# Performance work log

Hardware: AMD Instinct MI355X
Metric: run time of the kernel (lower is better)

Reference implementation:

```python
import jax, jax.numpy as jnp
import numpy as np

# Hyperparameters (from init_kwargs)
D_MODEL = 1024
D_STATE = 64
HEADDIM = 64
MIMO_RANK = 2
CHUNK = 128
EXPAND = 2
D_INNER = EXPAND * D_MODEL            # 2048
NHEADS = D_INNER // HEADDIM           # 32
G = MIMO_RANK * D_STATE               # effective state channels per head = 128
D_CONV = 4
D_XBC = D_INNER + 2 * NHEADS * G      # conv channels
D_IN_PROJ = 2 * D_INNER + 2 * NHEADS * G + NHEADS  # [z, x, B, C, dt]


def rmsnorm(x, w, eps=1e-5):
    return x * w * jax.lax.rsqrt(jnp.mean(x * x, axis=-1, keepdims=True) + eps)


def setup_inputs() -> dict:
    key = jax.random.key(0)
    ks = jax.random.split(key, 8)
    B, L = 2, 2048
    x = jax.random.normal(ks[0], (B, L, D_MODEL), jnp.float32)
    norm_w = jnp.ones((D_MODEL,), jnp.float32)
    in_proj_w = jax.random.normal(ks[1], (D_IN_PROJ, D_MODEL), jnp.float32) * 0.02
    conv_w = jax.random.normal(ks[2], (D_XBC, D_CONV), jnp.float32) * 0.2
    conv_b = jnp.zeros((D_XBC,), jnp.float32)
    dt_bias = jax.random.uniform(ks[3], (NHEADS,), jnp.float32, minval=-4.0, maxval=-1.0)
    A_log = jnp.log(jax.random.uniform(ks[4], (NHEADS,), jnp.float32, minval=1.0, maxval=8.0))
    D_skip = jnp.ones((NHEADS,), jnp.float32)
    gnorm_w = jnp.ones((D_INNER,), jnp.float32)
    out_proj_w = jax.random.normal(ks[5], (D_MODEL, D_INNER), jnp.float32) * 0.02
    return dict(x=x, norm_w=norm_w, in_proj_w=in_proj_w, conv_w=conv_w, conv_b=conv_b,
                dt_bias=dt_bias, A_log=A_log, D_skip=D_skip, gnorm_w=gnorm_w,
                out_proj_w=out_proj_w)


def _mamba3(u, in_proj_w, conv_w, conv_b, dt_bias, A_log, D_skip, gnorm_w, out_proj_w):
    B, L, _ = u.shape
    H, P = NHEADS, HEADDIM
    nc = L // CHUNK

    zxbcdt = u @ in_proj_w.T                                   # (B,L,D_IN_PROJ)
    z, xbc, dt_raw = jnp.split(zxbcdt, [D_INNER, D_INNER + D_XBC], axis=-1)

    # causal depthwise conv (width D_CONV) + SiLU on [x, B, C]
    xp = jnp.pad(xbc, ((0, 0), (D_CONV - 1, 0), (0, 0)))
    conv = conv_b + sum(xp[:, k:k + L, :] * conv_w[:, k] for k in range(D_CONV))
    xbc = jax.nn.silu(conv)
    xh, Bm, Cm = jnp.split(xbc, [D_INNER, D_INNER + H * G], axis=-1)

    Xc = xh.reshape(B, nc, CHUNK, H, P)
    Bc = Bm.reshape(B, nc, CHUNK, H, G)
    Cc = Cm.reshape(B, nc, CHUNK, H, G)

    dt = jax.nn.softplus(dt_raw + dt_bias)                     # (B,L,H), positive
    A = -jnp.exp(A_log)                                        # (H,), negative
    dtc = dt.reshape(B, nc, CHUNK, H)
    a = dtc * A                                                # log decay, (B,nc,cs,H)
    cum = jnp.cumsum(a, axis=2)                                # inclusive cumsum within chunk

    # intra-chunk (quadratic, causal) part
    cumT = cum.transpose(0, 1, 3, 2)                           # (B,nc,H,cs)
    diff = cumT[..., :, None] - cumT[..., None, :]             # cum_l - cum_s
    mask = jnp.tril(jnp.ones((CHUNK, CHUNK), bool))
    decay = jnp.where(mask, jnp.exp(jnp.where(mask, diff, 0.0)), 0.0)
    dtT = dtc.transpose(0, 1, 3, 2)                            # (B,nc,H,cs)
    scores = jnp.einsum('bclhg,bcshg->bchls', Cc, Bc) * decay * dtT[:, :, :, None, :]
    Y_intra = jnp.einsum('bchls,bcshp->bclhp', scores, Xc)

    # inter-chunk state recurrence
    w = jnp.exp(cum[:, :, -1:, :] - cum) * dtc                 # (B,nc,cs,H)
    S = jnp.einsum('bcshg,bcshp->bchgp', Bc * w[..., None], Xc)  # chunk states
    dlast = jnp.exp(cum[:, :, -1, :])                          # (B,nc,H) total chunk decay

    def step(carry, inp):
        dl, s = inp
        return dl[:, :, None, None] * carry + s, carry

    init = jnp.zeros((B, H, G, P), u.dtype)
    _, Hprev = jax.lax.scan(step, init, (dlast.transpose(1, 0, 2), S.transpose(1, 0, 2, 3, 4)))
    Hprev = Hprev.transpose(1, 0, 2, 3, 4)                     # (B,nc,H,G,P) state before chunk
    Y_inter = jnp.einsum('bclhg,bchgp->bclhp', Cc * jnp.exp(cum)[..., None], Hprev)

    y = (Y_intra + Y_inter + D_skip[:, None] * Xc).reshape(B, L, D_INNER)
    y = rmsnorm(y * jax.nn.silu(z), gnorm_w)                   # gated RMSNorm
    return y @ out_proj_w.T


def reference(x, norm_w, in_proj_w, conv_w, conv_b, dt_bias, A_log, D_skip, gnorm_w, out_proj_w):
    # pre-norm residual wrapper
    return x + _mamba3(rmsnorm(x, norm_w), in_proj_w, conv_w, conv_b,
                       dt_bias, A_log, D_skip, gnorm_w, out_proj_w)
```

## Files before the change

kernel.cpp:

```cpp
#include <hip/hip_runtime.h>

typedef unsigned short u16;
typedef __attribute__((ext_vector_type(8))) short bf16x8;
typedef __attribute__((ext_vector_type(4))) float f32x4;

#define MFMA16(a,b,c) __builtin_amdgcn_mfma_f32_16x16x32_bf16(a,b,c,0,0,0)

#define DMODEL   1024
#define DINNER   2048
#define NHEADS   32
#define HEADDIM  64
#define GDIM     128
#define DXBC     10240
#define DPROJ    12320
#define CHUNK_L  128
#define NCHUNK   16
#define NROWS    4096

__device__ __forceinline__ float b2f(u16 u){ return __uint_as_float(((unsigned)u)<<16); }
__device__ __forceinline__ u16 f2b(float f){
  unsigned u = __float_as_uint(f);
  u += 0x7fffu + ((u>>16)&1u);
  return (u16)(u>>16);
}

__device__ __forceinline__ void gload_lds16(const void* g, void* l){
  __builtin_amdgcn_global_load_lds(
      (const __attribute__((address_space(1))) unsigned int*)g,
      (__attribute__((address_space(3))) unsigned int*)l, 16, 0, 0);
}

__global__ void k_f32_to_bf16(const float* __restrict__ src, u16* __restrict__ dst, int n){
  int i = blockIdx.x*blockDim.x + threadIdx.x;
  int stride = gridDim.x*blockDim.x;
  int n4 = n >> 2;
  for (int j=i; j<n4; j+=stride){
    float4 v = reinterpret_cast<const float4*>(src)[j];
    uint2 o;
    o.x = (unsigned)f2b(v.x) | ((unsigned)f2b(v.y)<<16);
    o.y = (unsigned)f2b(v.z) | ((unsigned)f2b(v.w)<<16);
    reinterpret_cast<uint2*>(dst)[j] = o;
  }
}

__global__ __launch_bounds__(256) void k_rmsnorm_in(const float* __restrict__ x,
                                                    const float* __restrict__ w,
                                                    u16* __restrict__ u){
  int row = blockIdx.x, tid = threadIdx.x;
  float4 v = reinterpret_cast<const float4*>(x + (size_t)row*DMODEL)[tid];
  float ss = v.x*v.x + v.y*v.y + v.z*v.z + v.w*v.w;
  #pragma unroll
  for (int off=32; off>0; off>>=1) ss += __shfl_down(ss, off, 64);
  __shared__ float red[4];
  if ((tid&63)==0) red[tid>>6] = ss;
  __syncthreads();
  float tot = red[0]+red[1]+red[2]+red[3];
  float sc = rsqrtf(tot/(float)DMODEL + 1e-5f);
  float4 wv = reinterpret_cast<const float4*>(w)[tid];
  uint2 o;
  o.x = (unsigned)f2b(v.x*wv.x*sc) | ((unsigned)f2b(v.y*wv.y*sc)<<16);
  o.y = (unsigned)f2b(v.z*wv.z*sc) | ((unsigned)f2b(v.w*wv.w*sc)<<16);
  reinterpret_cast<uint2*>(u + (size_t)row*DMODEL)[tid] = o;
}

__global__ __launch_bounds__(512) void k_gemm1_8p(const u16* __restrict__ A,
                                                  const u16* __restrict__ W,
                                                  u16* __restrict__ zb,
                                                  u16* __restrict__ xbc){
  __shared__ __align__(16) u16 lds[65536];
  const int tid  = threadIdx.x;
  const int lane = tid & 63, w = tid >> 6;
  const int wr = w >> 2, wc = w & 3;
  int bid = blockIdx.x;
  int xcd = bid & 7, g = bid >> 3;
  int st  = xcd*6 + (g >> 4);
  int wi  = g & 15;
  int tm  = (st/12)*4 + (wi>>2);
  int tn  = (st%12)*4 + (wi&3);
  const int m0 = tm*256, n0 = tn*256;

  const int srow = w*8 + (lane>>3);
  const int scol = ((lane&7) ^ ((lane>>3)&7))*8;
  const u16* aS = A + (size_t)(m0 + srow)*DMODEL + scol;
  const u16* bS = W + (size_t)(n0 + srow)*DMODEL + scol;
  const int ldsw = w*512;

  const int rr = lane & 15, gq = lane >> 4;

  f32x4 acc[8][4];
  #pragma unroll
  for (int i=0;i<8;i++)
    #pragma unroll
    for (int j=0;j<4;j++) acc[i][j] = (f32x4){0,0,0,0};

  auto SU_A = [&](int kt, int j){
    gload_lds16(aS + (size_t)(j*64)*DMODEL + kt*64,
                lds + (kt&1)*32768 + j*4096 + ldsw);
  };
  auto SU_B = [&](int kt, int j){
    gload_lds16(bS + (size_t)(j*64)*DMODEL + kt*64,
                lds + (kt&1)*32768 + 16384 + j*4096 + ldsw);
  };

  SU_A(0,0); SU_A(0,2); SU_B(0,0); SU_B(0,2); SU_B(0,1); SU_B(0,3); SU_A(0,1); SU_A(0,3);
  asm volatile("s_waitcnt vmcnt(2)" ::: "memory");
  __builtin_amdgcn_s_barrier();
  __builtin_amdgcn_sched_barrier(0);

  for (int kt = 0; kt < 16; ++kt){
    const u16* bufA = lds + (kt&1)*32768;
    const u16* bufB = bufA + 16384;
    const bool stg = (kt < 15);
    bf16x8 af[4][2], bw0[2][2], bw1[2][2];

    auto RDA = [&](int ti, int ks)->bf16x8{
      int r = wr*128 + ti*16 + rr;
      int s = (ks*4 + gq) ^ (rr & 7);
      return *(const bf16x8*)&bufA[r*64 + s*8];
    };
    auto RDB = [&](int tj, int ks)->bf16x8{
      int r = wc*64 + tj*16 + rr;
      int s = (ks*4 + gq) ^ (rr & 7);
      return *(const bf16x8*)&bufB[r*64 + s*8];
    };

    #pragma unroll
    for (int ti=0;ti<4;ti++){ af[ti][0]=RDA(ti,0); af[ti][1]=RDA(ti,1); }
    #pragma unroll
    for (int tj=0;tj<2;tj++){ bw0[tj][0]=RDB(tj,0); bw0[tj][1]=RDB(tj,1); }
    if (stg){ SU_A(kt+1,0); SU_A(kt+1,2); }
    __builtin_amdgcn_s_barrier();
    asm volatile("s_waitcnt lgkmcnt(0)" ::: "memory");
    __builtin_amdgcn_sched_barrier(0);
    __builtin_amdgcn_s_setprio(1);
    #pragma unroll
    for (int ti=0;ti<4;ti++)
      #pragma unroll
      for (int tj=0;tj<2;tj++){
        acc[ti][tj] = MFMA16(af[ti][0], bw0[tj][0], acc[ti][tj]);
        acc[ti][tj] = MFMA16(af[ti][1], bw0[tj][1], acc[ti][tj]);
      }
    __builtin_amdgcn_s_setprio(0);
    __builtin_amdgcn_s_barrier();

    #pragma unroll
    for (int tj=0;tj<2;tj++){ bw1[tj][0]=RDB(tj+2,0); bw1[tj][1]=RDB(tj+2,1); }
    if (stg){ SU_B(kt+1,0); SU_B(kt+1,2); }
    __builtin_amdgcn_s_barrier();
    asm volatile("s_waitcnt lgkmcnt(0)" ::: "memory");
    __builtin_amdgcn_sched_barrier(0);
    __builtin_amdgcn_s_setprio(1);
    #pragma unroll
    for (int ti=0;ti<4;ti++)
      #pragma unroll
      for (int tj=0;tj<2;tj++){
        acc[ti][tj+2] = MFMA16(af[ti][0], bw1[tj][0], acc[ti][tj+2]);
        acc[ti][tj+2] = MFMA16(af[ti][1], bw1[tj][1], acc[ti][tj+2]);
      }
    __builtin_amdgcn_s_setprio(0);
    if (stg) asm volatile("s_waitcnt vmcnt(4)" ::: "memory");
    else     asm volatile("s_waitcnt vmcnt(0)" ::: "memory");
    __builtin_amdgcn_s_barrier();

    #pragma unroll
    for (int ti=0;ti<4;ti++){ af[ti][0]=RDA(ti+4,0); af[ti][1]=RDA(ti+4,1); }
    if (stg){ SU_B(kt+1,1); SU_B(kt+1,3); }
    __builtin_amdgcn_s_barrier();
    asm volatile("s_waitcnt lgkmcnt(0)" ::: "memory");
    __builtin_amdgcn_sched_barrier(0);
    __builtin_amdgcn_s_setprio(1);
    #pragma unroll
    for (int ti=0;ti<4;ti++)
      #pragma unroll
      for (int tj=0;tj<2;tj++){
        acc[4+ti][tj] = MFMA16(af[ti][0], bw0[tj][0], acc[4+ti][tj]);
        acc[4+ti][tj] = MFMA16(af[ti][1], bw0[tj][1], acc[4+ti][tj]);
      }
    __builtin_amdgcn_s_setprio(0);
    __builtin_amdgcn_s_barrier();

    if (stg){ SU_A(kt+1,1); SU_A(kt+1,3); }
    __builtin_amdgcn_s_barrier();
    __builtin_amdgcn_sched_barrier(0);
    __builtin_amdgcn_s_setprio(1);
    #pragma unroll
    for (int ti=0;ti<4;ti++)
      #pragma unroll
      for (int tj=0;tj<2;tj++){
        acc[4+ti][tj+2] = MFMA16(af[ti][0], bw1[tj][0], acc[4+ti][tj+2]);
        acc[4+ti][tj+2] = MFMA16(af[ti][1], bw1[tj][1], acc[4+ti][tj+2]);
      }
    __builtin_amdgcn_s_setprio(0);
    if (stg){
      asm volatile("s_waitcnt vmcnt(2)" ::: "memory");
      __builtin_amdgcn_s_barrier();
      __builtin_amdgcn_sched_barrier(0);
    }
  }

  const int row0 = m0 + wr*128 + (lane>>4)*4;
  const int colb = wc*64 + (lane&15);
  if (tn >= 8){
    const int cb = n0 - DINNER;
    #pragma unroll
    for (int ti=0;ti<8;ti++)
      #pragma unroll
      for (int tj=0;tj<4;tj++)
        #pragma unroll
        for (int q=0;q<4;q++)
          xbc[(size_t)(row0 + ti*16 + q)*DXBC + cb + colb + tj*16] = f2b(acc[ti][tj][q]);
  } else {
    #pragma unroll
    for (int ti=0;ti<8;ti++)
      #pragma unroll
      for (int tj=0;tj<4;tj++)
        #pragma unroll
        for (int q=0;q<4;q++)
          zb[(size_t)(row0 + ti*16 + q)*DINNER + n0 + colb + tj*16] = f2b(acc[ti][tj][q]);
  }
}

__global__ __launch_bounds__(256) void k_gemm_dt(const u16* __restrict__ A,
                                                 const u16* __restrict__ W,
                                                 float* __restrict__ dtraw){
  const int lane = threadIdx.x & 63, wv = threadIdx.x >> 6;
  const int m0 = blockIdx.x*32;
  const int n0 = DINNER + DXBC;
  const int r  = lane & 15;
  const int kb = (lane>>4)*8;
  const int k0 = wv*256;
  const u16* a0p = A + (size_t)(m0 + r)*DMODEL + k0 + kb;
  const u16* a1p = a0p + 16*DMODEL;
  const u16* b0p = W + (size_t)(n0 + r)*DMODEL + k0 + kb;
  const u16* b1p = b0p + 16*DMODEL;
  f32x4 acc00={0,0,0,0}, acc01={0,0,0,0}, acc10={0,0,0,0}, acc11={0,0,0,0};
  #pragma unroll
  for (int k=0;k<256;k+=32){
    bf16x8 a0 = *(const bf16x8*)(a0p + k);
    bf16x8 a1 = *(const bf16x8*)(a1p + k);
    bf16x8 b0 = *(const bf16x8*)(b0p + k);
    bf16x8 b1 = *(const bf16x8*)(b1p + k);
    acc00 = MFMA16(a0,b0,acc00);
    acc01 = MFMA16(a0,b1,acc01);
    acc10 = MFMA16(a1,b0,acc10);
    acc11 = MFMA16(a1,b1,acc11);
  }
  __shared__ float part[4][1024];
  int rowb = (lane>>4)*4, col = lane&15;
  #pragma unroll
  for (int rr=0; rr<4; rr++){
    part[wv][(rowb+rr)*32 + col]         = acc00[rr];
    part[wv][(rowb+rr)*32 + col+16]      = acc01[rr];
    part[wv][(rowb+16+rr)*32 + col]      = acc10[rr];
    part[wv][(rowb+16+rr)*32 + col+16]   = acc11[rr];
  }
  __syncthreads();
  int idx = threadIdx.x*4;
  #pragma unroll
  for (int q=0;q<4;q++){
    int i = idx+q;
    dtraw[(size_t)m0*NHEADS + i] = part[0][i]+part[1][i]+part[2][i]+part[3][i];
  }
}

__global__ __launch_bounds__(256) void k_conv(const u16* __restrict__ xbc,
                                              const float* __restrict__ cw,
                                              const float* __restrict__ cb,
                                              u16* __restrict__ xh,
                                              u16* __restrict__ Bm,
                                              u16* __restrict__ Cm){
  int c  = (blockIdx.x*256 + threadIdx.x)*2;
  int row0 = blockIdx.y*8;
  int l0 = row0 & 2047;
  float4 wa = reinterpret_cast<const float4*>(cw)[c];
  float4 wb = reinterpret_cast<const float4*>(cw)[c+1];
  float cba = cb[c], cbb = cb[c+1];
  float a3=0,a2=0,a1=0, b3=0,b2=0,b1=0;
  auto loadpair = [&](int rw, float& fa, float& fb){
    unsigned v = *(const unsigned*)&xbc[(size_t)rw*DXBC + c];
    fa = b2f((u16)v); fb = b2f((u16)(v>>16));
  };
  if (l0 >= 3){
    loadpair(row0-3, a3,b3); loadpair(row0-2, a2,b2); loadpair(row0-1, a1,b1);
  }
  #pragma unroll
  for (int i=0;i<8;i++){
    float a0,b0; loadpair(row0+i, a0,b0);
    float sa = cba + a3*wa.x + a2*wa.y + a1*wa.z + a0*wa.w;
    float sb = cbb + b3*wb.x + b2*wb.y + b1*wb.z + b0*wb.w;
    sa = sa/(1.f+expf(-sa)); sb = sb/(1.f+expf(-sb));
    unsigned o = (unsigned)f2b(sa) | ((unsigned)f2b(sb)<<16);
    int rw = row0 + i;
    if (c < DINNER)            *(unsigned*)&xh[(size_t)rw*DINNER + c] = o;
    else if (c < DINNER+4096)  *(unsigned*)&Bm[(size_t)rw*4096 + (c-DINNER)] = o;
    else                       *(unsigned*)&Cm[(size_t)rw*4096 + (c-DINNER-4096)] = o;
    a3=a2; a2=a1; a1=a0; b3=b2; b2=b1; b1=b0;
  }
}

__global__ __launch_bounds__(128) void k_dtscan(const float* __restrict__ dtraw,
                                                const float* __restrict__ dt_bias,
                                                const float* __restrict__ A_log,
                                                float* __restrict__ dtT,
                                                float* __restrict__ cumT){
  int blk = blockIdx.x;
  int h   = blk & 31;
  int bc  = blk >> 5;
  int s   = threadIdx.x;
  int row = bc*128 + s;
  float xv = dtraw[(size_t)row*NHEADS + h] + dt_bias[h];
  float dt = (xv > 20.f) ? xv : log1pf(expf(xv));
  float a  = dt * (-expf(A_log[h]));
  __shared__ float lds[128];
  lds[s] = a; __syncthreads();
  #pragma unroll
  for (int off=1; off<128; off<<=1){
    float t = (s>=off) ? lds[s-off] : 0.f;
    __syncthreads();
    lds[s] += t;
    __syncthreads();
  }
  dtT[(size_t)blk*128 + s]  = dt;
  cumT[(size_t)blk*128 + s] = lds[s];
}

__global__ __launch_bounds__(256) void k_states(const u16* __restrict__ Bm,
                                                const u16* __restrict__ xh,
                                                const float* __restrict__ dtT,
                                                const float* __restrict__ cumT,
                                                u16* __restrict__ S){
  int blk = blockIdx.x;
  int h = blk & 31, bc = blk >> 5;
  __shared__ __align__(16) u16 Bw[128][136];
  __shared__ __align__(16) u16 XT[64][136];
  __shared__ float cum[128], dtv[128];
  int tid = threadIdx.x;
  if (tid < 128){ cum[tid] = cumT[(size_t)blk*128+tid]; dtv[tid] = dtT[(size_t)blk*128+tid]; }
  __syncthreads();
  float clast = cum[127];
  #pragma unroll
  for (int it=0; it<8; ++it){
    int s  = it*16 + (tid>>4);
    int g8 = (tid&15)*8;
    uint4 v = *(const uint4*)&Bm[(size_t)(bc*128+s)*4096 + h*128 + g8];
    float w = expf(clast - cum[s]) * dtv[s];
    const u16* pv = (const u16*)&v;
    #pragma unroll
    for (int j=0;j<8;j++) Bw[g8+j][s] = f2b(b2f(pv[j]) * w);
  }
  #pragma unroll
  for (int it=0; it<8; ++it){
    int s  = it*16 + (tid>>4);
    int p4 = (tid&15)*4;
    uint2 v = *(const uint2*)&xh[(size_t)(bc*128+s)*DINNER + h*64 + p4];
    const u16* pv = (const u16*)&v;
    #pragma unroll
    for (int j=0;j<4;j++) XT[p4+j][s] = pv[j];
  }
  __syncthreads();
  int lane = tid & 63, wv = tid >> 6;
  int r = lane & 15, kb = (lane>>4)*8;
  f32x4 acc[2][4];
  #pragma unroll
  for (int i=0;i<2;i++)
    #pragma unroll
    for (int j=0;j<4;j++) acc[i][j] = (f32x4){0,0,0,0};
  #pragma unroll
  for (int k=0;k<128;k+=32){
    bf16x8 a0 = *(const bf16x8*)&Bw[wv*32 + r][k+kb];
    bf16x8 a1 = *(const bf16x8*)&Bw[wv*32 + 16 + r][k+kb];
    #pragma unroll
    for (int tj=0;tj<4;tj++){
      bf16x8 bb = *(const bf16x8*)&XT[tj*16 + r][k+kb];
      acc[0][tj] = MFMA16(a0,bb,acc[0][tj]);
      acc[1][tj] = MFMA16(a1,bb,acc[1][tj]);
    }
  }
  u16* Sp = S + (size_t)blk*8192;
  int g0 = wv*32 + (lane>>4)*4, p0 = lane&15;
  #pragma unroll
  for (int ti=0;ti<2;ti++)
    #pragma unroll
    for (int tj=0;tj<4;tj++)
      #pragma unroll
      for (int rr=0;rr<4;rr++)
        Sp[(g0 + ti*16 + rr)*64 + tj*16 + p0] = f2b(acc[ti][tj][rr]);
}

__global__ __launch_bounds__(256) void k_scan(const u16* __restrict__ S,
                                              const float* __restrict__ cumT,
                                              u16* __restrict__ Hp){
  int slice = blockIdx.x & 3;
  int bh = blockIdx.x >> 2;
  int b = bh >> 5, h = bh & 31;
  int e0 = slice*2048 + threadIdx.x*8;
  float c8[8];
  #pragma unroll
  for (int j=0;j<8;j++) c8[j] = 0.f;
  for (int c=0;c<NCHUNK;c++){
    int blk = (b*16+c)*32 + h;
    float dl = expf(cumT[(size_t)blk*128 + 127]);
    uint4 sv = *(const uint4*)&S[(size_t)blk*8192 + e0];
    const u16* sp = (const u16*)&sv;
    uint4 o; u16* op = (u16*)&o;
    #pragma unroll
    for (int j=0;j<8;j++) op[j] = f2b(c8[j]);
    *reinterpret_cast<uint4*>(&Hp[(size_t)blk*8192 + e0]) = o;
    #pragma unroll
    for (int j=0;j<8;j++) c8[j] = dl*c8[j] + b2f(sp[j]);
  }
}

__global__ __launch_bounds__(256) void k_intra(const u16* __restrict__ Cm,
                                               const u16* __restrict__ Bm,
                                               const u16* __restrict__ xh,
                                               const u16* __restrict__ Hp,
                                               const float* __restrict__ dtT,
                                               const float* __restrict__ cumT,
                                               const float* __restrict__ Dskip,
                                               u16* __restrict__ yh){
  int blk = blockIdx.x;
  int h = blk & 31, bc = blk >> 5;
  __shared__ __align__(16) u16 Cl[128][136];
  __shared__ __align__(16) u16 Bl[128][136];
  __shared__ __align__(16) u16 XT[64][136];
  __shared__ __align__(16) u16 HT[64][136];
  __shared__ float cum[128], dtv[128];
  int tid = threadIdx.x;
  if (tid < 128){ cum[tid] = cumT[(size_t)blk*128+tid]; dtv[tid] = dtT[(size_t)blk*128+tid]; }
  #pragma unroll
  for (int it=0; it<8; ++it){
    int rw = it*16 + (tid>>4);
    int g8 = (tid&15)*8;
    *(uint4*)&Cl[rw][g8] = *(const uint4*)&Cm[(size_t)(bc*128+rw)*4096 + h*128 + g8];
    *(uint4*)&Bl[rw][g8] = *(const uint4*)&Bm[(size_t)(bc*128+rw)*4096 + h*128 + g8];
  }
  #pragma unroll
  for (int it=0; it<8; ++it){
    int s  = it*16 + (tid>>4);
    int p4 = (tid&15)*4;
    uint2 v = *(const uint2*)&xh[(size_t)(bc*128+s)*DINNER + h*64 + p4];
    const u16* pv = (const u16*)&v;
    #pragma unroll
    for (int j=0;j<4;j++) XT[p4+j][s] = pv[j];
  }
  #pragma unroll
  for (int it=0; it<8; ++it){
    int g  = it*16 + (tid>>4);
    int p4 = (tid&15)*4;
    uint2 v = *(const uint2*)&Hp[(size_t)blk*8192 + g*64 + p4];
    const u16* pv = (const u16*)&v;
    #pragma unroll
    for (int j=0;j<4;j++) HT[p4+j][g] = pv[j];
  }
  __syncthreads();
  int lane = tid & 63, wv = tid >> 6;
  int r = lane & 15, kb = (lane>>4)*8;
  const int tjmax = 2*wv + 1;

  f32x4 p1[2][8];
  #pragma unroll
  for (int i=0;i<2;i++)
    #pragma unroll
    for (int j=0;j<8;j++) p1[i][j] = (f32x4){0,0,0,0};
  #pragma unroll
  for (int k=0;k<128;k+=32){
    bf16x8 a0 = *(const bf16x8*)&Cl[wv*32 + r][k+kb];
    bf16x8 a1 = *(const bf16x8*)&Cl[wv*32 + 16 + r][k+kb];
    #pragma unroll
    for (int tj=0;tj<8;tj++){
      if (tj > tjmax) continue;
      bf16x8 bb = *(const bf16x8*)&Bl[tj*16 + r][k+kb];
      p1[0][tj] = MFMA16(a0,bb,p1[0][tj]);
      p1[1][tj] = MFMA16(a1,bb,p1[1][tj]);
    }
  }
  __syncthreads();
  int row0 = wv*32 + (lane>>4)*4;
  #pragma unroll
  for (int ti=0;ti<2;ti++)
    #pragma unroll
    for (int tj=0;tj<8;tj++)
      #pragma unroll
      for (int rr=0;rr<4;rr++){
        int l = row0 + ti*16 + rr;
        int s = tj*16 + (lane&15);
        float v = p1[ti][tj][rr];
        v = (s <= l) ? v * expf(cum[l]-cum[s]) * dtv[s] : 0.f;
        Bl[l][s] = f2b(v);
      }
  __syncthreads();

  f32x4 y[2][4];
  #pragma unroll
  for (int i=0;i<2;i++)
    #pragma unroll
    for (int j=0;j<4;j++) y[i][j] = (f32x4){0,0,0,0};
  #pragma unroll
  for (int k=0;k<128;k+=32){
    bf16x8 a0 = *(const bf16x8*)&Cl[wv*32 + r][k+kb];
    bf16x8 a1 = *(const bf16x8*)&Cl[wv*32 + 16 + r][k+kb];
    #pragma unroll
    for (int tj=0;tj<4;tj++){
      bf16x8 bb = *(const bf16x8*)&HT[tj*16 + r][k+kb];
      y[0][tj] = MFMA16(a0,bb,y[0][tj]);
      y[1][tj] = MFMA16(a1,bb,y[1][tj]);
    }
  }
  #pragma unroll
  for (int ti=0;ti<2;ti++){
    #pragma unroll
    for (int rr=0;rr<4;rr++){
      float e = expf(cum[row0 + ti*16 + rr]);
      #pragma unroll
      for (int tj=0;tj<4;tj++) y[ti][tj][rr] *= e;
    }
  }
  #pragma unroll
  for (int k=0;k<128;k+=32){
    bf16x8 a0 = *(const bf16x8*)&Bl[wv*32 + r][k+kb];
    bf16x8 a1 = *(const bf16x8*)&Bl[wv*32 + 16 + r][k+kb];
    #pragma unroll
    for (int tj=0;tj<4;tj++){
      bf16x8 bb = *(const bf16x8*)&XT[tj*16 + r][k+kb];
      y[0][tj] = MFMA16(a0,bb,y[0][tj]);
      y[1][tj] = MFMA16(a1,bb,y[1][tj]);
    }
  }
  float Dh = Dskip[h];
  #pragma unroll
  for (int ti=0;ti<2;ti++)
    #pragma unroll
    for (int tj=0;tj<4;tj++)
      #pragma unroll
      for (int rr=0;rr<4;rr++){
        int l = row0 + ti*16 + rr;
        int p = tj*16 + (lane&15);
        float xv = b2f(XT[p][l]);
        yh[(size_t)(bc*128 + l)*DINNER + h*64 + p] = f2b(y[ti][tj][rr] + Dh*xv);
      }
}

__global__ __launch_bounds__(256) void k_gate(const u16* __restrict__ yh,
                                              const u16* __restrict__ zb,
                                              const float* __restrict__ gw,
                                              u16* __restrict__ out){
  int row = blockIdx.x, tid = threadIdx.x;
  const uint4 yv = reinterpret_cast<const uint4*>(yh + (size_t)row*DINNER)[tid];
  const uint4 zv = reinterpret_cast<const uint4*>(zb + (size_t)row*DINNER)[tid];
  const unsigned* yp = (const unsigned*)&yv;
  const unsigned* zp = (const unsigned*)&zv;
  float t[8]; float ss = 0.f;
  #pragma unroll
  for (int i=0;i<4;i++){
    float y0 = b2f((u16)yp[i]), y1 = b2f((u16)(yp[i]>>16));
    float z0 = b2f((u16)zp[i]), z1 = b2f((u16)(zp[i]>>16));
    float v0 = y0 * (z0 / (1.f + expf(-z0)));
    float v1 = y1 * (z1 / (1.f + expf(-z1)));
    t[2*i] = v0; t[2*i+1] = v1; ss += v0*v0 + v1*v1;
  }
  #pragma unroll
  for (int off=32; off>0; off>>=1) ss += __shfl_down(ss, off, 64);
  __shared__ float red[4];
  if ((tid&63)==0) red[tid>>6] = ss;
  __syncthreads();
  float tot = red[0]+red[1]+red[2]+red[3];
  float g = rsqrtf(tot/(float)DINNER + 1e-5f);
  const float4 g0 = reinterpret_cast<const float4*>(gw)[tid*2];
  const float4 g1 = reinterpret_cast<const float4*>(gw)[tid*2+1];
  uint4 o;
  unsigned* op = (unsigned*)&o;
  float gg[8] = {g0.x,g0.y,g0.z,g0.w,g1.x,g1.y,g1.z,g1.w};
  #pragma unroll
  for (int i=0;i<4;i++)
    op[i] = (unsigned)f2b(t[2*i]*gg[2*i]*g) | ((unsigned)f2b(t[2*i+1]*gg[2*i+1]*g)<<16);
  reinterpret_cast<uint4*>(out + (size_t)row*DINNER)[tid] = o;
}

__global__ __launch_bounds__(256) void k_gemm2_db(const u16* __restrict__ A,
                                                  const u16* __restrict__ W,
                                                  const float* __restrict__ xres,
                                                  float* __restrict__ out){
  __shared__ __align__(16) u16 lds[2*8192];
  const int tid  = threadIdx.x;
  const int lane = tid & 63, wv = tid >> 6;
  const int wr = wv >> 1, wc = wv & 1;
  const int NWG = 8*32, Q = NWG/8;
  int swz = (blockIdx.x & 7)*Q + (blockIdx.x >> 3);
  int tm = swz / 8, tn = swz % 8;
  int m0 = tm*128, n0 = tn*128;

  const int K = DINNER;
  const int srcslot = ((lane&3) ^ ((lane>>3)&3)) * 8;
  const u16* aS0 = A + (size_t)(m0 + wv*32 + (lane>>2))*K + srcslot;
  const u16* aS1 = aS0 + (size_t)16*K;
  const u16* bS0 = W + (size_t)(n0 + wv*32 + (lane>>2))*K + srcslot;
  const u16* bS1 = bS0 + (size_t)16*K;
  const int ldsW = (wv*32)*32;
  const int rr = lane & 15;
  const int kb = (((lane>>4) ^ ((lane>>1)&3))) * 8;

  f32x4 acc[4][4];
  #pragma unroll
  for (int i=0;i<4;i++)
    #pragma unroll
    for (int j=0;j<4;j++) acc[i][j] = (f32x4){0,0,0,0};

  int stage_off = 0;
  auto STAGE = [&](int ks){
    u16* base = lds + (ks&1)*8192;
    gload_lds16(aS0 + stage_off, base + ldsW);
    gload_lds16(aS1 + stage_off, base + 16*32 + ldsW);
    gload_lds16(bS0 + stage_off, base + 4096 + ldsW);
    gload_lds16(bS1 + stage_off, base + 4096 + 16*32 + ldsW);
    stage_off += 32;
  };
  auto KSTEP = [&](int ks, int stage_ks){
    const u16* As = lds + (ks&1)*8192;
    const u16* Bs = As + 4096;
    bf16x8 af[4], bw[4];
    #pragma unroll
    for (int t=0;t<4;t++){
      af[t] = *(const bf16x8*)&As[(wr*64 + t*16 + rr)*32 + kb];
      bw[t] = *(const bf16x8*)&Bs[(wc*64 + t*16 + rr)*32 + kb];
    }
    asm volatile("s_waitcnt lgkmcnt(0)" ::: "memory");
    __builtin_amdgcn_s_barrier();
    if (stage_ks >= 0) STAGE(stage_ks);
    __builtin_amdgcn_s_setprio(1);
    #pragma unroll
    for (int ti=0;ti<4;ti++)
      #pragma unroll
      for (int tj=0;tj<4;tj++)
        acc[ti][tj] = MFMA16(af[ti], bw[tj], acc[ti][tj]);
    __builtin_amdgcn_s_setprio(0);
  };

  STAGE(0); STAGE(1);
  asm volatile("s_waitcnt vmcnt(4)" ::: "memory");
  __builtin_amdgcn_s_barrier();
  __builtin_amdgcn_sched_barrier(0);
  const int NK = K/32;
  for (int ks = 0; ks < NK-2; ++ks){
    KSTEP(ks, ks+2);
    asm volatile("s_waitcnt vmcnt(4)" ::: "memory");
    __builtin_amdgcn_s_barrier();
    __builtin_amdgcn_sched_barrier(0);
  }
  KSTEP(NK-2, -1);
  asm volatile("s_waitcnt vmcnt(0)" ::: "memory");
  __builtin_amdgcn_s_barrier();
  __builtin_amdgcn_sched_barrier(0);
  KSTEP(NK-1, -1);

  int row0 = m0 + wr*64 + (lane>>4)*4;
  int col0 = n0 + wc*64 + (lane&15);
  #pragma unroll
  for (int ti=0;ti<4;ti++)
    #pragma unroll
    for (int tj=0;tj<4;tj++)
      #pragma unroll
      for (int q=0;q<4;q++){
        size_t idx = (size_t)(row0+ti*16+q)*DMODEL + col0 + tj*16;
        out[idx] = acc[ti][tj][q] + xres[idx];
      }
}

extern "C" void kernel_launch(void* const* d_in, const int* in_sizes, int n_in,
                              void* d_out, int out_size, void* d_ws, size_t ws_size,
                              hipStream_t stream) {
  (void)in_sizes; (void)n_in; (void)out_size; (void)ws_size;
  const float* x         = (const float*)d_in[0];
  const float* norm_w    = (const float*)d_in[1];
  const float* in_proj_w = (const float*)d_in[2];
  const float* conv_w    = (const float*)d_in[3];
  const float* conv_b    = (const float*)d_in[4];
  const float* dt_bias   = (const float*)d_in[5];
  const float* A_log     = (const float*)d_in[6];
  const float* D_skip    = (const float*)d_in[7];
  const float* gnorm_w   = (const float*)d_in[8];
  const float* out_proj_w= (const float*)d_in[9];
  float* out = (float*)d_out;

  char* ws = (char*)d_ws;
  size_t off = 0;
  auto alloc = [&](size_t bytes)->char*{
    char* p = ws + off; off = (off + bytes + 255) & ~(size_t)255; return p;
  };
  u16*   W2    = (u16*)  alloc((size_t)DMODEL*DINNER*2);
  u16*   zb    = (u16*)  alloc((size_t)NROWS*DINNER*2);
  float* dtraw = (float*)alloc((size_t)NROWS*NHEADS*4);
  float* dtT   = (float*)alloc((size_t)1024*128*4);
  float* cumT  = (float*)alloc((size_t)1024*128*4);
  u16*   xhb   = (u16*)  alloc((size_t)NROWS*DINNER*2);
  u16*   Bmb   = (u16*)  alloc((size_t)NROWS*4096*2);
  u16*   Cmb   = (u16*)  alloc((size_t)NROWS*4096*2);
  char*  R1    = alloc((size_t)NROWS*DXBC*2);
  u16*   xbcr  = (u16*)R1;
  u16*   S     = (u16*)R1;
  u16*   Hp    = (u16*)(R1 + (size_t)1024*8192*4);
  u16*   yh    = (u16*)R1;
  char*  R2    = alloc((size_t)DPROJ*DMODEL*2 + (size_t)NROWS*DMODEL*2);
  u16*   W1    = (u16*)R2;
  u16*   u_bf  = (u16*)(R2 + (size_t)DPROJ*DMODEL*2);
  u16*   gated = (u16*)R2;

  k_f32_to_bf16<<<2048,256,0,stream>>>(in_proj_w, W1, DPROJ*DMODEL);
  k_f32_to_bf16<<<512,256,0,stream>>>(out_proj_w, W2, DMODEL*DINNER);
  k_rmsnorm_in<<<NROWS,256,0,stream>>>(x, norm_w, u_bf);
  k_gemm1_8p<<<768,512,0,stream>>>(u_bf, W1, zb, xbcr);
  k_gemm_dt<<<NROWS/32,256,0,stream>>>(u_bf, W1, dtraw);
  k_conv<<<dim3(DXBC/512, NROWS/8),256,0,stream>>>(xbcr, conv_w, conv_b, xhb, Bmb, Cmb);
  k_dtscan<<<1024,128,0,stream>>>(dtraw, dt_bias, A_log, dtT, cumT);
  k_states<<<1024,256,0,stream>>>(Bmb, xhb, dtT, cumT, S);
  k_scan<<<256,256,0,stream>>>(S, cumT, Hp);
  k_intra<<<1024,256,0,stream>>>(Cmb, Bmb, xhb, Hp, dtT, cumT, D_skip, yh);
  k_gate<<<NROWS,256,0,stream>>>(yh, zb, gnorm_w, gated);
  k_gemm2_db<<<8*32,256,0,stream>>>(gated, W2, x, out);
}
```

Before: 307.8 us.

## Fold dt projection into gemm1, merge weight casts, widen SSM kernels to 512 threads

The two weight-conversion launches are merged into one kernel, and the dt projection GEMM becomes 8 extra blocks appended to the main in-projection GEMM launch. Each of those blocks does the full K loop per wave, so the old cross-wave LDS reduction is gone. k_states and k_intra now use 512 threads with 16 rows per wave instead of 32, giving more waves per block and fewer registers per wave. The aim is to cut launch overhead and raise occupancy in the chunked SSM kernels. The trade-offs are a small tail in gemm1 from the extra dt blocks and lower per-wave MFMA reuse in the widened kernels.

After: 339.7 us. 1.1x slower.

```diff
diff --git a/kernel.cpp b/kernel.cpp
--- a/kernel.cpp
+++ b/kernel.cpp
@@ -30,16 +30,20 @@
       (__attribute__((address_space(3))) unsigned int*)l, 16, 0, 0);
 }
 
-__global__ void k_f32_to_bf16(const float* __restrict__ src, u16* __restrict__ dst, int n){
+__global__ void k_f32_to_bf16_2(const float* __restrict__ s1, u16* __restrict__ d1, int n1,
+                                const float* __restrict__ s2, u16* __restrict__ d2, int n2){
   int i = blockIdx.x*blockDim.x + threadIdx.x;
   int stride = gridDim.x*blockDim.x;
-  int n4 = n >> 2;
-  for (int j=i; j<n4; j+=stride){
-    float4 v = reinterpret_cast<const float4*>(src)[j];
+  int t1 = n1 >> 2, t2 = n2 >> 2;
+  for (int j=i; j<t1+t2; j+=stride){
+    const float4* sp; uint2* dp; int idx;
+    if (j < t1){ sp = (const float4*)s1; dp = (uint2*)d1; idx = j; }
+    else       { sp = (const float4*)s2; dp = (uint2*)d2; idx = j - t1; }
+    float4 v = sp[idx];
     uint2 o;
     o.x = (unsigned)f2b(v.x) | ((unsigned)f2b(v.y)<<16);
     o.y = (unsigned)f2b(v.z) | ((unsigned)f2b(v.w)<<16);
-    reinterpret_cast<uint2*>(dst)[j] = o;
+    dp[idx] = o;
   }
 }
 
@@ -66,10 +70,50 @@
 __global__ __launch_bounds__(512) void k_gemm1_8p(const u16* __restrict__ A,
                                                   const u16* __restrict__ W,
                                                   u16* __restrict__ zb,
-                                                  u16* __restrict__ xbc){
+                                                  u16* __restrict__ xbc,
+                                                  float* __restrict__ dtraw){
   __shared__ __align__(16) u16 lds[65536];
   const int tid  = threadIdx.x;
   const int lane = tid & 63, w = tid >> 6;
+
+  if (blockIdx.x >= 768){
+    const int m0 = (blockIdx.x - 768)*512 + w*64;
+    const int r  = lane & 15, kb = (lane>>4)*8;
+    const u16* ap0 = A + (size_t)(m0 +  0 + r)*DMODEL + kb;
+    const u16* ap1 = A + (size_t)(m0 + 16 + r)*DMODEL + kb;
+    const u16* ap2 = A + (size_t)(m0 + 32 + r)*DMODEL + kb;
+    const u16* ap3 = A + (size_t)(m0 + 48 + r)*DMODEL + kb;
+    const u16* b0p = W + (size_t)(12288 + r)*DMODEL + kb;
+    const u16* b1p = b0p + (size_t)16*DMODEL;
+    f32x4 acc[4][2];
+    #pragma unroll
+    for (int t=0;t<4;t++){ acc[t][0]=(f32x4){0,0,0,0}; acc[t][1]=(f32x4){0,0,0,0}; }
+    #pragma unroll 4
+    for (int k=0;k<DMODEL;k+=32){
+      bf16x8 b0 = *(const bf16x8*)(b0p + k);
+      bf16x8 b1 = *(const bf16x8*)(b1p + k);
+      bf16x8 a0 = *(const bf16x8*)(ap0 + k);
+      bf16x8 a1 = *(const bf16x8*)(ap1 + k);
+      bf16x8 a2 = *(const bf16x8*)(ap2 + k);
+      bf16x8 a3 = *(const bf16x8*)(ap3 + k);
+      acc[0][0] = MFMA16(a0,b0,acc[0][0]); acc[0][1] = MFMA16(a0,b1,acc[0][1]);
+      acc[1][0] = MFMA16(a1,b0,acc[1][0]); acc[1][1] = MFMA16(a1,b1,acc[1][1]);
+      acc[2][0] = MFMA16(a2,b0,acc[2][0]); acc[2][1] = MFMA16(a2,b1,acc[2][1]);
+      acc[3][0] = MFMA16(a3,b0,acc[3][0]); acc[3][1] = MFMA16(a3,b1,acc[3][1]);
+    }
+    const int col = lane & 15;
+    #pragma unroll
+    for (int t=0;t<4;t++){
+      int rowb = m0 + t*16 + (lane>>4)*4;
+      #pragma unroll
+      for (int q=0;q<4;q++){
+        dtraw[(size_t)(rowb+q)*NHEADS + col]      = acc[t][0][q];
+        dtraw[(size_t)(rowb+q)*NHEADS + col+16]   = acc[t][1][q];
+      }
+    }
+    return;
+  }
+
   const int wr = w >> 2, wc = w & 3;
   int bid = blockIdx.x;
   int xcd = bid & 7, g = bid >> 3;
@@ -217,49 +261,6 @@
         #pragma unroll
         for (int q=0;q<4;q++)
           zb[(size_t)(row0 + ti*16 + q)*DINNER + n0 + colb + tj*16] = f2b(acc[ti][tj][q]);
-  }
-}
-
-__global__ __launch_bounds__(256) void k_gemm_dt(const u16* __restrict__ A,
-                                                 const u16* __restrict__ W,
-                                                 float* __restrict__ dtraw){
-  const int lane = threadIdx.x & 63, wv = threadIdx.x >> 6;
-  const int m0 = blockIdx.x*32;
-  const int n0 = DINNER + DXBC;
-  const int r  = lane & 15;
-  const int kb = (lane>>4)*8;
-  const int k0 = wv*256;
-  const u16* a0p = A + (size_t)(m0 + r)*DMODEL + k0 + kb;
-  const u16* a1p = a0p + 16*DMODEL;
-  const u16* b0p = W + (size_t)(n0 + r)*DMODEL + k0 + kb;
-  const u16* b1p = b0p + 16*DMODEL;
-  f32x4 acc00={0,0,0,0}, acc01={0,0,0,0}, acc10={0,0,0,0}, acc11={0,0,0,0};
-  #pragma unroll
-  for (int k=0;k<256;k+=32){
-    bf16x8 a0 = *(const bf16x8*)(a0p + k);
-    bf16x8 a1 = *(const bf16x8*)(a1p + k);
-    bf16x8 b0 = *(const bf16x8*)(b0p + k);
-    bf16x8 b1 = *(const bf16x8*)(b1p + k);
-    acc00 = MFMA16(a0,b0,acc00);
-    acc01 = MFMA16(a0,b1,acc01);
-    acc10 = MFMA16(a1,b0,acc10);
-    acc11 = MFMA16(a1,b1,acc11);
-  }
-  __shared__ float part[4][1024];
-  int rowb = (lane>>4)*4, col = lane&15;
-  #pragma unroll
-  for (int rr=0; rr<4; rr++){
-    part[wv][(rowb+rr)*32 + col]         = acc00[rr];
-    part[wv][(rowb+rr)*32 + col+16]      = acc01[rr];
-    part[wv][(rowb+16+rr)*32 + col]      = acc10[rr];
-    part[wv][(rowb+16+rr)*32 + col+16]   = acc11[rr];
-  }
-  __syncthreads();
-  int idx = threadIdx.x*4;
-  #pragma unroll
-  for (int q=0;q<4;q++){
-    int i = idx+q;
-    dtraw[(size_t)m0*NHEADS + i] = part[0][i]+part[1][i]+part[2][i]+part[3][i];
   }
 }
 
@@ -324,7 +325,7 @@
   cumT[(size_t)blk*128 + s] = lds[s];
 }
 
-__global__ __launch_bounds__(256) void k_states(const u16* __restrict__ Bm,
+__global__ __launch_bounds__(512) void k_states(const u16* __restrict__ Bm,
                                                 const u16* __restrict__ xh,
                                                 const float* __restrict__ dtT,
                                                 const float* __restrict__ cumT,
@@ -339,8 +340,8 @@
   __syncthreads();
   float clast = cum[127];
   #pragma unroll
-  for (int it=0; it<8; ++it){
-    int s  = it*16 + (tid>>4);
+  for (int it=0; it<4; ++it){
+    int s  = it*32 + (tid>>4);
     int g8 = (tid&15)*8;
     uint4 v = *(const uint4*)&Bm[(size_t)(bc*128+s)*4096 + h*128 + g8];
     float w = expf(clast - cum[s]) * dtv[s];
@@ -349,8 +350,8 @@
     for (int j=0;j<8;j++) Bw[g8+j][s] = f2b(b2f(pv[j]) * w);
   }
   #pragma unroll
-  for (int it=0; it<8; ++it){
-    int s  = it*16 + (tid>>4);
+  for (int it=0; it<4; ++it){
+    int s  = it*32 + (tid>>4);
     int p4 = (tid&15)*4;
     uint2 v = *(const uint2*)&xh[(size_t)(bc*128+s)*DINNER + h*64 + p4];
     const u16* pv = (const u16*)&v;
@@ -360,31 +361,25 @@
   __syncthreads();
   int lane = tid & 63, wv = tid >> 6;
   int r = lane & 15, kb = (lane>>4)*8;
-  f32x4 acc[2][4];
-  #pragma unroll
-  for (int i=0;i<2;i++)
-    #pragma unroll
-    for (int j=0;j<4;j++) acc[i][j] = (f32x4){0,0,0,0};
+  f32x4 acc[4];
+  #pragma unroll
+  for (int j=0;j<4;j++) acc[j] = (f32x4){0,0,0,0};
   #pragma unroll
   for (int k=0;k<128;k+=32){
-    bf16x8 a0 = *(const bf16x8*)&Bw[wv*32 + r][k+kb];
-    bf16x8 a1 = *(const bf16x8*)&Bw[wv*32 + 16 + r][k+kb];
+    bf16x8 a0 = *(const bf16x8*)&Bw[wv*16 + r][k+kb];
     #pragma unroll
     for (int tj=0;tj<4;tj++){
       bf16x8 bb = *(const bf16x8*)&XT[tj*16 + r][k+kb];
-      acc[0][tj] = MFMA16(a0,bb,acc[0][tj]);
-      acc[1][tj] = MFMA16(a1,bb,acc[1][tj]);
+      acc[tj] = MFMA16(a0,bb,acc[tj]);
     }
   }
   u16* Sp = S + (size_t)blk*8192;
-  int g0 = wv*32 + (lane>>4)*4, p0 = lane&15;
-  #pragma unroll
-  for (int ti=0;ti<2;ti++)
-    #pragma unroll
-    for (int tj=0;tj<4;tj++)
-      #pragma unroll
-      for (int rr=0;rr<4;rr++)
-        Sp[(g0 + ti*16 + rr)*64 + tj*16 + p0] = f2b(acc[ti][tj][rr]);
+  int g0 = wv*16 + (lane>>4)*4, p0 = lane&15;
+  #pragma unroll
+  for (int tj=0;tj<4;tj++)
+    #pragma unroll
+    for (int rr=0;rr<4;rr++)
+      Sp[(g0 + rr)*64 + tj*16 + p0] = f2b(acc[tj][rr]);
 }
 
 __global__ __launch_bounds__(256) void k_scan(const u16* __restrict__ S,
@@ -411,7 +406,7 @@
   }
 }
 
-__global__ __launch_bounds__(256) void k_intra(const u16* __restrict__ Cm,
+__global__ __launch_bounds__(512) void k_intra(const u16* __restrict__ Cm,
                                                const u16* __restrict__ Bm,
                                                const u16* __restrict__ xh,
                                                const u16* __restrict__ Hp,
@@ -429,15 +424,15 @@
   int tid = threadIdx.x;
   if (tid < 128){ cum[tid] = cumT[(size_t)blk*128+tid]; dtv[tid] = dtT[(size_t)blk*128+tid]; }
   #pragma unroll
-  for (int it=0; it<8; ++it){
-    int rw = it*16 + (tid>>4);
+  for (int it=0; it<4; ++it){
+    int rw = it*32 + (tid>>4);
     int g8 = (tid&15)*8;
     *(uint4*)&Cl[rw][g8] = *(const uint4*)&Cm[(size_t)(bc*128+rw)*4096 + h*128 + g8];
     *(uint4*)&Bl[rw][g8] = *(const uint4*)&Bm[(size_t)(bc*128+rw)*4096 + h*128 + g8];
   }
   #pragma unroll
-  for (int it=0; it<8; ++it){
-    int s  = it*16 + (tid>>4);
+  for (int it=0; it<4; ++it){
+    int s  = it*32 + (tid>>4);
     int p4 = (tid&15)*4;
     uint2 v = *(const uint2*)&xh[(size_t)(bc*128+s)*DINNER + h*64 + p4];
     const u16* pv = (const u16*)&v;
@@ -445,8 +440,8 @@
     for (int j=0;j<4;j++) XT[p4+j][s] = pv[j];
   }
   #pragma unroll
-  for (int it=0; it<8; ++it){
-    int g  = it*16 + (tid>>4);
+  for (int it=0; it<4; ++it){
+    int g  = it*32 + (tid>>4);
     int p4 = (tid&15)*4;
     uint2 v = *(const uint2*)&Hp[(size_t)blk*8192 + g*64 + p4];
     const u16* pv = (const u16*)&v;
@@ -456,89 +451,72 @@
   __syncthreads();
   int lane = tid & 63, wv = tid >> 6;
   int r = lane & 15, kb = (lane>>4)*8;
-  const int tjmax = 2*wv + 1;
-
-  f32x4 p1[2][8];
-  #pragma unroll
-  for (int i=0;i<2;i++)
-    #pragma unroll
-    for (int j=0;j<8;j++) p1[i][j] = (f32x4){0,0,0,0};
+  const int tjmax = wv;
+
+  f32x4 p1[8];
+  #pragma unroll
+  for (int j=0;j<8;j++) p1[j] = (f32x4){0,0,0,0};
   #pragma unroll
   for (int k=0;k<128;k+=32){
-    bf16x8 a0 = *(const bf16x8*)&Cl[wv*32 + r][k+kb];
-    bf16x8 a1 = *(const bf16x8*)&Cl[wv*32 + 16 + r][k+kb];
+    bf16x8 a0 = *(const bf16x8*)&Cl[wv*16 + r][k+kb];
     #pragma unroll
     for (int tj=0;tj<8;tj++){
       if (tj > tjmax) continue;
       bf16x8 bb = *(const bf16x8*)&Bl[tj*16 + r][k+kb];
-      p1[0][tj] = MFMA16(a0,bb,p1[0][tj]);
-      p1[1][tj] = MFMA16(a1,bb,p1[1][tj]);
+      p1[tj] = MFMA16(a0,bb,p1[tj]);
     }
   }
   __syncthreads();
-  int row0 = wv*32 + (lane>>4)*4;
-  #pragma unroll
-  for (int ti=0;ti<2;ti++)
-    #pragma unroll
-    for (int tj=0;tj<8;tj++)
-      #pragma unroll
-      for (int rr=0;rr<4;rr++){
-        int l = row0 + ti*16 + rr;
-        int s = tj*16 + (lane&15);
-        float v = p1[ti][tj][rr];
-        v = (s <= l) ? v * expf(cum[l]-cum[s]) * dtv[s] : 0.f;
-        Bl[l][s] = f2b(v);
-      }
+  int row0 = wv*16 + (lane>>4)*4;
+  #pragma unroll
+  for (int tj=0;tj<8;tj++)
+    #pragma unroll
+    for (int rr=0;rr<4;rr++){
+      int l = row0 + rr;
+      int s = tj*16 + (lane&15);
+      float v = p1[tj][rr];
+      v = (s <= l) ? v * expf(cum[l]-cum[s]) * dtv[s] : 0.f;
+      Bl[l][s] = f2b(v);
+    }
   __syncthreads();
 
-  f32x4 y[2][4];
-  #pragma unroll
-  for (int i=0;i<2;i++)
-    #pragma unroll
-    for (int j=0;j<4;j++) y[i][j] = (f32x4){0,0,0,0};
+  f32x4 y[4];
+  #pragma unroll
+  for (int j=0;j<4;j++) y[j] = (f32x4){0,0,0,0};
   #pragma unroll
   for (int k=0;k<128;k+=32){
-    bf16x8 a0 = *(const bf16x8*)&Cl[wv*32 + r][k+kb];
-    bf16x8 a1 = *(const bf16x8*)&Cl[wv*32 + 16 + r][k+kb];
+    bf16x8 a0 = *(const bf16x8*)&Cl[wv*16 + r][k+kb];
     #pragma unroll
     for (int tj=0;tj<4;tj++){
       bf16x8 bb = *(const bf16x8*)&HT[tj*16 + r][k+kb];
-      y[0][tj] = MFMA16(a0,bb,y[0][tj]);
-      y[1][tj] = MFMA16(a1,bb,y[1][tj]);
-    }
-  }
-  #pragma unroll
-  for (int ti=0;ti<2;ti++){
-    #pragma unroll
-    for (int rr=0;rr<4;rr++){
-      float e = expf(cum[row0 + ti*16 + rr]);
-      #pragma unroll
-      for (int tj=0;tj<4;tj++) y[ti][tj][rr] *= e;
-    }
+      y[tj] = MFMA16(a0,bb,y[tj]);
+    }
+  }
+  #pragma unroll
+  for (int rr=0;rr<4;rr++){
+    float e = expf(cum[row0 + rr]);
+    #pragma unroll
+    for (int tj=0;tj<4;tj++) y[tj][rr] *= e;
   }
   #pragma unroll
   for (int k=0;k<128;k+=32){
-    bf16x8 a0 = *(const bf16x8*)&Bl[wv*32 + r][k+kb];
-    bf16x8 a1 = *(const bf16x8*)&Bl[wv*32 + 16 + r][k+kb];
+    bf16x8 a0 = *(const bf16x8*)&Bl[wv*16 + r][k+kb];
     #pragma unroll
     for (int tj=0;tj<4;tj++){
       bf16x8 bb = *(const bf16x8*)&XT[tj*16 + r][k+kb];
-      y[0][tj] = MFMA16(a0,bb,y[0][tj]);
-      y[1][tj] = MFMA16(a1,bb,y[1][tj]);
+      y[tj] = MFMA16(a0,bb,y[tj]);
     }
   }
   float Dh = Dskip[h];
   #pragma unroll
-  for (int ti=0;ti<2;ti++)
-    #pragma unroll
-    for (int tj=0;tj<4;tj++)
-      #pragma unroll
-      for (int rr=0;rr<4;rr++){
-        int l = row0 + ti*16 + rr;
-        int p = tj*16 + (lane&15);
-        float xv = b2f(XT[p][l]);
-        yh[(size_t)(bc*128 + l)*DINNER + h*64 + p] = f2b(y[ti][tj][rr] + Dh*xv);
-      }
+  for (int tj=0;tj<4;tj++)
+    #pragma unroll
+    for (int rr=0;rr<4;rr++){
+      int l = row0 + rr;
+      int p = tj*16 + (lane&15);
+      float xv = b2f(XT[p][l]);
+      yh[(size_t)(bc*128 + l)*DINNER + h*64 + p] = f2b(y[tj][rr] + Dh*xv);
+    }
 }
 
 __global__ __launch_bounds__(256) void k_gate(const u16* __restrict__ yh,
@@ -705,16 +683,15 @@
   u16*   u_bf  = (u16*)(R2 + (size_t)DPROJ*DMODEL*2);
   u16*   gated = (u16*)R2;
 
-  k_f32_to_bf16<<<2048,256,0,stream>>>(in_proj_w, W1, DPROJ*DMODEL);
-  k_f32_to_bf16<<<512,256,0,stream>>>(out_proj_w, W2, DMODEL*DINNER);
+  k_f32_to_bf16_2<<<2048,256,0,stream>>>(in_proj_w, W1, DPROJ*DMODEL,
+                                         out_proj_w, W2, DMODEL*DINNER);
   k_rmsnorm_in<<<NROWS,256,0,stream>>>(x, norm_w, u_bf);
-  k_gemm1_8p<<<768,512,0,stream>>>(u_bf, W1, zb, xbcr);
-  k_gemm_dt<<<NROWS/32,256,0,stream>>>(u_bf, W1, dtraw);
+  k_gemm1_8p<<<776,512,0,stream>>>(u_bf, W1, zb, xbcr, dtraw);
   k_conv<<<dim3(DXBC/512, NROWS/8),256,0,stream>>>(xbcr, conv_w, conv_b, xhb, Bmb, Cmb);
   k_dtscan<<<1024,128,0,stream>>>(dtraw, dt_bias, A_log, dtT, cumT);
-  k_states<<<1024,256,0,stream>>>(Bmb, xhb, dtT, cumT, S);
+  k_states<<<1024,512,0,stream>>>(Bmb, xhb, dtT, cumT, S);
   k_scan<<<256,256,0,stream>>>(S, cumT, Hp);
-  k_intra<<<1024,256,0,stream>>>(Cmb, Bmb, xhb, Hp, dtT, cumT, D_skip, yh);
+  k_intra<<<1024,512,0,stream>>>(Cmb, Bmb, xhb, Hp, dtT, cumT, D_skip, yh);
   k_gate<<<NROWS,256,0,stream>>>(yh, zb, gnorm_w, gated);
   k_gemm2_db<<<8*32,256,0,stream>>>(gated, W2, x, out);
 }
```
